# Performance work log

Hardware: AMD Instinct MI355X
Metric: run time of the kernel (lower is better)

The kernel has to match this reference:

```python
import jax, jax.numpy as jnp
import numpy as np

N_DOCS = 500000
N_WORDS = 100000
EMB = 128
B = 16384
CTX = 8
K = 6


def setup_inputs() -> dict:
    key = jax.random.key(0)
    k1, k2, k3, k4, k5, k6 = jax.random.split(key, 6)
    D = jax.random.normal(k1, (N_DOCS, EMB), dtype=jnp.float32)
    # W = cat(randn(n_words, d), zeros(1, d)) -> last row is padding
    W = jax.random.normal(k2, (N_WORDS + 1, EMB), dtype=jnp.float32)
    W = W.at[-1].set(0.0)
    Wp = jax.random.normal(k3, (EMB, N_WORDS), dtype=jnp.float32)
    ctx_ids = jax.random.randint(k4, (B, CTX), 0, N_WORDS + 1, dtype=jnp.int64)
    doc_ids = jax.random.randint(k5, (B,), 0, N_DOCS, dtype=jnp.int64)
    target_and_noise_ids = jax.random.randint(k6, (B, K), 0, N_WORDS, dtype=jnp.int64)
    return {
        "D": D,
        "W": W,
        "Wp": Wp,
        "ctx_ids": ctx_ids,
        "doc_ids": doc_ids,
        "target_and_noise_ids": target_and_noise_ids,
    }


def reference(D, W, Wp, ctx_ids, doc_ids, target_and_noise_ids):
    # x[b] = D[doc_ids[b]] + sum_c W[ctx_ids[b, c]]      -> [B, d]
    x = D[doc_ids] + jnp.sum(W[ctx_ids], axis=1)
    # out[b, k] = x[b] . Wp[:, target_and_noise_ids[b, k]]
    # Wp.T[ids] gathers rows of Wp.T -> [B, K, d]
    out = jnp.einsum("bd,bkd->bk", x, Wp.T[target_and_noise_ids])
    return out
```

## Files before the change

kernel.cpp:

```cpp
#include <hip/hip_runtime.h>

#define N_DOCS 500000
#define N_WORDS 100000
#define EMB 128
#define BATCH 16384
#define CTX 8
#define K 6

__device__ __forceinline__ unsigned short f2bf(float f) {
    unsigned u = __float_as_uint(f);
    unsigned r = u + 0x7fffu + ((u >> 16) & 1u);
    return (unsigned short)(r >> 16);
}
#define BF2F(h) __uint_as_float(((unsigned)(h)) << 16)

__global__ __launch_bounds__(256) void transpose_bf16(const float* __restrict__ Wp,
                                                      unsigned short* __restrict__ WpT) {
    __shared__ float tile[32][33];
    const int ctile = blockIdx.x;
    const int rtile = blockIdx.y;
    const int tx = threadIdx.x;
    const int ty = threadIdx.y;

    const int col = ctile * 32 + tx;
#pragma unroll
    for (int j = 0; j < 4; ++j) {
        const int row = rtile * 32 + ty + j * 8;
        tile[ty + j * 8][tx] = Wp[(size_t)row * N_WORDS + col];
    }
    __syncthreads();
#pragma unroll
    for (int j = 0; j < 4; ++j) {
        const int r = ty + j * 8;
        WpT[(size_t)(ctile * 32 + r) * EMB + rtile * 32 + tx] = f2bf(tile[tx][r]);
    }
}

__global__ __launch_bounds__(256) void nce_fused(const float* __restrict__ D,
                                                 const float* __restrict__ W,
                                                 const unsigned short* __restrict__ WpT,
                                                 const int* __restrict__ ctx_ids,
                                                 const int* __restrict__ doc_ids,
                                                 const int* __restrict__ tn_ids,
                                                 float* __restrict__ out) {
    const int lane = threadIdx.x & 63;
    const int b = __builtin_amdgcn_readfirstlane(blockIdx.x * 4 + (threadIdx.x >> 6));

    const int doc = doc_ids[b];
    float2 xx = ((const float2*)(D + (size_t)doc * EMB))[lane];
#pragma unroll
    for (int c = 0; c < CTX; ++c) {
        const int id = ctx_ids[b * CTX + c];
        const float2 w2 = ((const float2*)(W + (size_t)id * EMB))[lane];
        xx.x += w2.x;
        xx.y += w2.y;
    }

#pragma unroll
    for (int k = 0; k < K; ++k) {
        const int id = tn_ids[b * K + k];
        const ushort2 w2 = ((const ushort2*)(WpT + (size_t)id * EMB))[lane];
        float s = xx.x * BF2F(w2.x) + xx.y * BF2F(w2.y);
#pragma unroll
        for (int off = 32; off > 0; off >>= 1) s += __shfl_xor(s, off, 64);
        if (lane == 0) out[b * K + k] = s;
    }
}

__global__ __launch_bounds__(256) void nce_direct(
    const float* __restrict__ D, const float* __restrict__ W,
    const float* __restrict__ Wp, const int* __restrict__ ctx_ids,
    const int* __restrict__ doc_ids, const int* __restrict__ tn_ids,
    float* __restrict__ out) {
    const int wave = threadIdx.x >> 6, lane = threadIdx.x & 63;
    const int b = blockIdx.x * 4 + wave;
    if (b >= BATCH) return;
    float2 xx = ((const float2*)(D + (size_t)doc_ids[b] * EMB))[lane];
#pragma unroll
    for (int c = 0; c < CTX; ++c) {
        const float2 w2 = ((const float2*)(W + (size_t)ctx_ids[b * CTX + c] * EMB))[lane];
        xx.x += w2.x;
        xx.y += w2.y;
    }
#pragma unroll
    for (int k = 0; k < K; ++k) {
        const int id = tn_ids[b * K + k];
        float s = xx.x * Wp[(size_t)(2 * lane) * N_WORDS + id] +
                  xx.y * Wp[(size_t)(2 * lane + 1) * N_WORDS + id];
#pragma unroll
        for (int off = 32; off > 0; off >>= 1) s += __shfl_down(s, off, 64);
        if (lane == 0) out[b * K + k] = s;
    }
}

extern "C" void kernel_launch(void* const* d_in, const int* in_sizes, int n_in,
                              void* d_out, int out_size, void* d_ws, size_t ws_size,
                              hipStream_t stream) {
    const float* D  = (const float*)d_in[0];
    const float* W  = (const float*)d_in[1];
    const float* Wp = (const float*)d_in[2];
    const int* ctx  = (const int*)d_in[3];
    const int* doc  = (const int*)d_in[4];
    const int* tn   = (const int*)d_in[5];
    float* out = (float*)d_out;

    const size_t need = (size_t)N_WORDS * EMB * sizeof(unsigned short);
    if (ws_size >= need) {
        unsigned short* WpT = (unsigned short*)d_ws;
        transpose_bf16<<<dim3(N_WORDS / 32, EMB / 32), dim3(32, 8), 0, stream>>>(Wp, WpT);
        nce_fused<<<BATCH / 4, 256, 0, stream>>>(D, W, WpT, ctx, doc, tn, out);
    } else {
        nce_direct<<<BATCH / 4, 256, 0, stream>>>(D, W, Wp, ctx, doc, tn, out);
    }
}
```

Before: 36.49 us.

## Overlap Wp transpose with x gather in one launch, split dot into per-pair waves

Merges the bf16 transpose of Wp and the computation of x = D[doc] + sum W[ctx] into one kernel, using block-index ranges so the two independent jobs run concurrently, and writes x to workspace. A second kernel then computes each (b,k) dot product with its own wavefront, giving six times more parallel waves for the dependent gathers. This aims to hide the x-gather latency behind the transpose and raise memory-level parallelism. In exchange it adds a round trip of x (8 MB) through global memory and each x row is reread six times.

```diff
diff --git a/kernel.cpp b/kernel.cpp
--- a/kernel.cpp
+++ b/kernel.cpp
@@ -6,6 +6,8 @@
 #define BATCH 16384
 #define CTX 8
 #define K 6
+#define TBLK 12500
+#define XBLK (BATCH / 4)
 
 __device__ __forceinline__ unsigned short f2bf(float f) {
     unsigned u = __float_as_uint(f);
@@ -14,57 +16,57 @@
 }
 #define BF2F(h) __uint_as_float(((unsigned)(h)) << 16)
 
-__global__ __launch_bounds__(256) void transpose_bf16(const float* __restrict__ Wp,
-                                                      unsigned short* __restrict__ WpT) {
-    __shared__ float tile[32][33];
-    const int ctile = blockIdx.x;
-    const int rtile = blockIdx.y;
-    const int tx = threadIdx.x;
-    const int ty = threadIdx.y;
-
-    const int col = ctile * 32 + tx;
+__global__ __launch_bounds__(256) void mega(const float* __restrict__ Wp,
+                                            unsigned short* __restrict__ WpT,
+                                            const float* __restrict__ D,
+                                            const float* __restrict__ W,
+                                            const int* __restrict__ ctx_ids,
+                                            const int* __restrict__ doc_ids,
+                                            float* __restrict__ x) {
+    const int bid = blockIdx.x;
+    if (bid < TBLK) {
+        __shared__ float tile[32][33];
+        const int ctile = bid % 3125;
+        const int rtile = bid / 3125;
+        const int tx = threadIdx.x & 31, ty = threadIdx.x >> 5;
+        const int col = ctile * 32 + tx;
 #pragma unroll
-    for (int j = 0; j < 4; ++j) {
-        const int row = rtile * 32 + ty + j * 8;
-        tile[ty + j * 8][tx] = Wp[(size_t)row * N_WORDS + col];
-    }
-    __syncthreads();
+        for (int j = 0; j < 4; ++j)
+            tile[ty + 8 * j][tx] = Wp[(size_t)(rtile * 32 + ty + 8 * j) * N_WORDS + col];
+        __syncthreads();
 #pragma unroll
-    for (int j = 0; j < 4; ++j) {
-        const int r = ty + j * 8;
-        WpT[(size_t)(ctile * 32 + r) * EMB + rtile * 32 + tx] = f2bf(tile[tx][r]);
+        for (int j = 0; j < 4; ++j) {
+            const int r = ty + 8 * j;
+            WpT[(size_t)(ctile * 32 + r) * EMB + rtile * 32 + tx] = f2bf(tile[tx][r]);
+        }
+    } else {
+        const int lane = threadIdx.x & 63;
+        const int b = __builtin_amdgcn_readfirstlane((bid - TBLK) * 4 + (threadIdx.x >> 6));
+        float2 xx = ((const float2*)(D + (size_t)doc_ids[b] * EMB))[lane];
+#pragma unroll
+        for (int c = 0; c < CTX; ++c) {
+            const float2 w2 = ((const float2*)(W + (size_t)ctx_ids[b * CTX + c] * EMB))[lane];
+            xx.x += w2.x;
+            xx.y += w2.y;
+        }
+        ((float2*)(x + (size_t)b * EMB))[lane] = xx;
     }
 }
 
-__global__ __launch_bounds__(256) void nce_fused(const float* __restrict__ D,
-                                                 const float* __restrict__ W,
-                                                 const unsigned short* __restrict__ WpT,
-                                                 const int* __restrict__ ctx_ids,
-                                                 const int* __restrict__ doc_ids,
-                                                 const int* __restrict__ tn_ids,
-                                                 float* __restrict__ out) {
+__global__ __launch_bounds__(256) void dotk(const unsigned short* __restrict__ WpT,
+                                            const float* __restrict__ x,
+                                            const int* __restrict__ tn,
+                                            float* __restrict__ out) {
     const int lane = threadIdx.x & 63;
-    const int b = __builtin_amdgcn_readfirstlane(blockIdx.x * 4 + (threadIdx.x >> 6));
-
-    const int doc = doc_ids[b];
-    float2 xx = ((const float2*)(D + (size_t)doc * EMB))[lane];
+    const int p = __builtin_amdgcn_readfirstlane(blockIdx.x * 4 + (threadIdx.x >> 6));
+    const int id = tn[p];
+    const int b = (int)((unsigned)p / 6u);
+    const float2 xv = ((const float2*)(x + (size_t)b * EMB))[lane];
+    const ushort2 w2 = ((const ushort2*)(WpT + (size_t)id * EMB))[lane];
+    float s = xv.x * BF2F(w2.x) + xv.y * BF2F(w2.y);
 #pragma unroll
-    for (int c = 0; c < CTX; ++c) {
-        const int id = ctx_ids[b * CTX + c];
-        const float2 w2 = ((const float2*)(W + (size_t)id * EMB))[lane];
-        xx.x += w2.x;
-        xx.y += w2.y;
-    }
-
-#pragma unroll
-    for (int k = 0; k < K; ++k) {
-        const int id = tn_ids[b * K + k];
-        const ushort2 w2 = ((const ushort2*)(WpT + (size_t)id * EMB))[lane];
-        float s = xx.x * BF2F(w2.x) + xx.y * BF2F(w2.y);
-#pragma unroll
-        for (int off = 32; off > 0; off >>= 1) s += __shfl_xor(s, off, 64);
-        if (lane == 0) out[b * K + k] = s;
-    }
+    for (int off = 32; off > 0; off >>= 1) s += __shfl_xor(s, off, 64);
+    if (lane == 0) out[p] = s;
 }
 
 __global__ __launch_bounds__(256) void nce_direct(
@@ -104,11 +106,15 @@
     const int* tn   = (const int*)d_in[5];
     float* out = (float*)d_out;
 
-    const size_t need = (size_t)N_WORDS * EMB * sizeof(unsigned short);
+    const size_t wpt_sz = (size_t)N_WORDS * EMB * sizeof(unsigned short);
+    const size_t x_off  = (wpt_sz + 255) & ~(size_t)255;
+    const size_t need   = x_off + (size_t)BATCH * EMB * sizeof(float);
+
     if (ws_size >= need) {
         unsigned short* WpT = (unsigned short*)d_ws;
-        transpose_bf16<<<dim3(N_WORDS / 32, EMB / 32), dim3(32, 8), 0, stream>>>(Wp, WpT);
-        nce_fused<<<BATCH / 4, 256, 0, stream>>>(D, W, WpT, ctx, doc, tn, out);
+        float* x = (float*)((char*)d_ws + x_off);
+        mega<<<TBLK + XBLK, 256, 0, stream>>>(Wp, WpT, D, W, ctx, doc, x);
+        dotk<<<BATCH * K / 4, 256, 0, stream>>>(WpT, x, tn, out);
     } else {
         nce_direct<<<BATCH / 4, 256, 0, stream>>>(D, W, Wp, ctx, doc, tn, out);
     }
```

New measurement: 44.95 us. 23.2% more time.
